# Performance work log

Hardware: AMD Instinct MI355X
Metric: run time of the kernel (lower is better)

## Reference

```python
import jax, jax.numpy as jnp
import numpy as np

N_QUBITS = 12
N_LAYERS = 2
LATENT = 4
BATCH = 8192


def setup_inputs() -> dict:
    key = jax.random.key(0)
    k1, k2, k3, k4, k5, k6 = jax.random.split(key, 6)
    inputs = jax.random.normal(k1, (BATCH, N_QUBITS), jnp.float32)
    q_params = jax.random.normal(k2, (N_LAYERS, N_QUBITS, 3), jnp.float32)
    W1 = jax.random.normal(k3, (32, LATENT), jnp.float32) * 0.3
    b1 = jax.random.normal(k4, (32,), jnp.float32) * 0.1
    W2 = jax.random.normal(k5, (N_QUBITS, 32), jnp.float32) * 0.2
    b2 = jax.random.normal(k6, (N_QUBITS,), jnp.float32) * 0.1
    return {"inputs": inputs, "q_params": q_params, "W1": W1, "b1": b1, "W2": W2, "b2": b2}


def _rot_matrix(phi, theta, omega):
    # PennyLane Rot(phi, theta, omega) = RZ(omega) @ RY(theta) @ RZ(phi)
    c = jnp.cos(theta / 2)
    s = jnp.sin(theta / 2)
    ep = jnp.exp(-0.5j * (phi + omega))  # e^{-i(phi+omega)/2}
    em = jnp.exp(-0.5j * (phi - omega))  # e^{-i(phi-omega)/2}
    row0 = jnp.stack([ep * c, -jnp.conj(em) * s])
    row1 = jnp.stack([em * s, jnp.conj(ep) * c])
    return jnp.stack([row0, row1]).astype(jnp.complex64)  # (2,2)


def _apply_1q(state, U, wire):
    # state: (B,) + (2,)*N_QUBITS ; U: (2,2) shared across batch
    ax = wire + 1
    state = jnp.moveaxis(state, ax, -1)
    state = jnp.einsum('ij,...j->...i', U, state)
    return jnp.moveaxis(state, -1, ax)


def _cnot(state, control, target):
    c_ax, t_ax = control + 1, target + 1
    s0 = jnp.take(state, jnp.array([0]), axis=c_ax)
    s1 = jnp.take(state, jnp.array([1]), axis=c_ax)
    s1 = jnp.flip(s1, axis=t_ax)  # X on target where control==1
    return jnp.concatenate([s0, s1], axis=c_ax)


def _z_expval(state, wire):
    p = state.real ** 2 + state.imag ** 2
    ax = wire + 1
    other = tuple(a for a in range(1, N_QUBITS + 1) if a != ax)
    pw = p.sum(axis=other)  # (B, 2)
    return pw[:, 0] - pw[:, 1]


def reference(inputs, q_params, W1, b1, W2, b2):
    B = inputs.shape[0]
    # Initial |0..0> state followed by per-wire RX(x_i): product state
    # RX(a)|0> = [cos(a/2), -i sin(a/2)]
    c = jnp.cos(inputs / 2).astype(jnp.complex64)  # (B, n)
    s = jnp.sin(inputs / 2).astype(jnp.complex64)
    qvec = jnp.stack([c, -1j * s], axis=-1)  # (B, n, 2)
    state = jnp.ones((B, 1), jnp.complex64)
    for i in range(N_QUBITS):
        state = (state[:, :, None] * qvec[:, i, None, :]).reshape(B, -1)
    state = state.reshape((B,) + (2,) * N_QUBITS)

    for l in range(N_LAYERS):
        for i in range(N_QUBITS):
            phi, theta, omega = q_params[l, i, 0], q_params[l, i, 1], q_params[l, i, 2]
            state = _apply_1q(state, _rot_matrix(phi, theta, omega), i)
        for i in range(N_QUBITS - 1):
            state = _cnot(state, i, i + 1)

    latents = jnp.stack([_z_expval(state, i) for i in range(LATENT)], axis=1)
    latents = latents.astype(jnp.float32)  # (B, latent)

    h = jax.nn.relu(latents @ W1.T + b1)
    return h @ W2.T + b2
```

## Files before the change

kernel.cpp:

```cpp
#include <hip/hip_runtime.h>
#include <hip/hip_bf16.h>


__device__ __forceinline__ void fsincos(float x, float& s, float& c) {
    s = __sinf(x);
    c = __cosf(x);
}

__global__ __launch_bounds__(64) void qae_kernel(
    const float* __restrict__ inputs,
    const float* __restrict__ qp,
    const float* __restrict__ W1,
    const float* __restrict__ b1,
    const float* __restrict__ W2,
    const float* __restrict__ b2,
    float* __restrict__ out,
    int B)
{
    int b = blockIdx.x * blockDim.x + threadIdx.x;
    if (b >= B) return;
    const float* x = inputs + (size_t)b * 12;

    float4 xv = *reinterpret_cast<const float4*>(x);
    float x4 = x[4];

    float cj[5], sj[5];
    fsincos(0.5f * xv.x, sj[0], cj[0]);
    fsincos(0.5f * xv.y, sj[1], cj[1]);
    fsincos(0.5f * xv.z, sj[2], cj[2]);
    fsincos(0.5f * xv.w, sj[3], cj[3]);
    fsincos(0.5f * x4,   sj[4], cj[4]);

    float sr[32], si[32];
#pragma unroll
    for (int idx = 0; idx < 32; ++idx) {
        float m = 1.0f;
#pragma unroll
        for (int j = 0; j < 5; ++j) m *= ((idx >> j) & 1) ? sj[j] : cj[j];
        int pc = __popc(idx) & 3;
        sr[idx] = (pc == 0) ? m : ((pc == 2) ? -m : 0.0f);
        si[idx] = (pc == 1) ? -m : ((pc == 3) ? m : 0.0f);
    }

#pragma unroll
    for (int l = 0; l < 2; ++l) {
#pragma unroll
        for (int w = 0; w < 5; ++w) {
            const float* p = qp + (l * 12 + w) * 3;
            float phi = p[0], th = p[1], om = p[2];
            float st, ct, sha, cha, shb, chb;
            fsincos(0.5f * th, st, ct);
            fsincos(0.5f * (phi + om), sha, cha);
            fsincos(0.5f * (phi - om), shb, chb);
            float u00r =  cha * ct, u00i = -sha * ct;
            float u01r = -chb * st, u01i = -shb * st;
            float u10r =  chb * st, u10i = -shb * st;
            float u11r =  cha * ct, u11i =  sha * ct;
#pragma unroll
            for (int k = 0; k < 16; ++k) {
                int i0 = ((k >> w) << (w + 1)) | (k & ((1 << w) - 1));
                int i1 = i0 | (1 << w);
                float a0r = sr[i0], a0i = si[i0];
                float a1r = sr[i1], a1i = si[i1];
                sr[i0] = u00r * a0r - u00i * a0i + u01r * a1r - u01i * a1i;
                si[i0] = u00r * a0i + u00i * a0r + u01r * a1i + u01i * a1r;
                sr[i1] = u10r * a0r - u10i * a0i + u11r * a1r - u11i * a1i;
                si[i1] = u10r * a0i + u10i * a0r + u11r * a1i + u11i * a1r;
            }
        }
#pragma unroll
        for (int cw = 0; cw < 4; ++cw) {
#pragma unroll
            for (int idx = 0; idx < 32; ++idx) {
                if (((idx >> cw) & 1) && !((idx >> (cw + 1)) & 1)) {
                    int j2 = idx | (1 << (cw + 1));
                    float tr = sr[idx]; sr[idx] = sr[j2]; sr[j2] = tr;
                    float ti = si[idx]; si[idx] = si[j2]; si[j2] = ti;
                }
            }
        }
    }

    float lat[4] = {0.f, 0.f, 0.f, 0.f};
#pragma unroll
    for (int idx = 0; idx < 32; ++idx) {
        float pr = sr[idx] * sr[idx] + si[idx] * si[idx];
#pragma unroll
        for (int q = 0; q < 4; ++q)
            lat[q] += ((idx >> q) & 1) ? -pr : pr;
    }

    float o[12];
#pragma unroll
    for (int j = 0; j < 12; ++j) o[j] = b2[j];
#pragma unroll
    for (int u = 0; u < 32; ++u) {
        float acc = b1[u];
#pragma unroll
        for (int i = 0; i < 4; ++i) acc += lat[i] * W1[u * 4 + i];
        float h = fmaxf(acc, 0.0f);
#pragma unroll
        for (int j = 0; j < 12; ++j) o[j] += h * W2[j * 32 + u];
    }

    float4* op = reinterpret_cast<float4*>(out + (size_t)b * 12);
    op[0] = make_float4(o[0], o[1], o[2], o[3]);
    op[1] = make_float4(o[4], o[5], o[6], o[7]);
    op[2] = make_float4(o[8], o[9], o[10], o[11]);
}

extern "C" void kernel_launch(void* const* d_in, const int* in_sizes, int n_in,
                              void* d_out, int out_size, void* d_ws, size_t ws_size,
                              hipStream_t stream) {
    const float* inputs = (const float*)d_in[0];
    const float* qp     = (const float*)d_in[1];
    const float* W1     = (const float*)d_in[2];
    const float* b1     = (const float*)d_in[3];
    const float* W2     = (const float*)d_in[4];
    const float* b2     = (const float*)d_in[5];
    float* out = (float*)d_out;

    int B = in_sizes[0] / 12;
    int block = 64;
    int grid = (B + block - 1) / block;
    qae_kernel<<<grid, block, 0, stream>>>(inputs, qp, W1, b1, W2, b2, out, B);
}
```

Measured before the change: 76.18 us.

## Split each 32-amplitude statevector across 8 lanes with shuffle-based gates

Each batch element's 32-amplitude reduced state is now distributed over 8 threads holding 4 amplitudes each. Gates on the high wires and the CNOT permutations become cross-lane __shfl_xor exchanges, and the latent reduction and MLP are split across the 8 lanes and combined with shuffle reductions. This cuts per-thread register use and raises the thread count from 8192 to 65536, aiming for better occupancy and latency hiding on a small grid. The cost is many extra shuffles and redundant sincos and parameter work in every lane.

```diff
diff --git a/kernel.cpp b/kernel.cpp
--- a/kernel.cpp
+++ b/kernel.cpp
@@ -7,7 +7,7 @@
     c = __cosf(x);
 }
 
-__global__ __launch_bounds__(64) void qae_kernel(
+__global__ __launch_bounds__(256) void qae_kernel(
     const float* __restrict__ inputs,
     const float* __restrict__ qp,
     const float* __restrict__ W1,
@@ -17,10 +17,12 @@
     float* __restrict__ out,
     int B)
 {
-    int b = blockIdx.x * blockDim.x + threadIdx.x;
-    if (b >= B) return;
-    const float* x = inputs + (size_t)b * 12;
+    int tid = blockIdx.x * blockDim.x + threadIdx.x;
+    int e   = tid >> 3;
+    int sub = tid & 7;
+    if (e >= B) return;
 
+    const float* x = inputs + (size_t)e * 12;
     float4 xv = *reinterpret_cast<const float4*>(x);
     float x4 = x[4];
 
@@ -31,15 +33,27 @@
     fsincos(0.5f * xv.w, sj[3], cj[3]);
     fsincos(0.5f * x4,   sj[4], cj[4]);
 
-    float sr[32], si[32];
+    float fsub = ((sub & 1) ? sj[2] : cj[2])
+               * ((sub & 2) ? sj[3] : cj[3])
+               * ((sub & 4) ? sj[4] : cj[4]);
+
+    float ar[4], ai[4];
 #pragma unroll
-    for (int idx = 0; idx < 32; ++idx) {
-        float m = 1.0f;
-#pragma unroll
-        for (int j = 0; j < 5; ++j) m *= ((idx >> j) & 1) ? sj[j] : cj[j];
-        int pc = __popc(idx) & 3;
-        sr[idx] = (pc == 0) ? m : ((pc == 2) ? -m : 0.0f);
-        si[idx] = (pc == 1) ? -m : ((pc == 3) ? m : 0.0f);
+    for (int r = 0; r < 4; ++r) {
+        float m = fsub * ((r & 1) ? sj[0] : cj[0]) * ((r & 2) ? sj[1] : cj[1]);
+        int pc = (__popc(sub) + __popc(r)) & 3;
+        ar[r] = (pc == 0) ? m : ((pc == 2) ? -m : 0.0f);
+        ai[r] = (pc == 1) ? -m : ((pc == 3) ? m : 0.0f);
+    }
+
+#define APPLY_PAIR(i0, i1)                                        \
+    {                                                             \
+        float a0r = ar[i0], a0i = ai[i0];                         \
+        float a1r = ar[i1], a1i = ai[i1];                         \
+        ar[i0] = u00r*a0r - u00i*a0i + u01r*a1r - u01i*a1i;       \
+        ai[i0] = u00r*a0i + u00i*a0r + u01r*a1i + u01i*a1r;       \
+        ar[i1] = u10r*a0r - u10i*a0i + u11r*a1r - u11i*a1i;       \
+        ai[i1] = u10r*a0i + u10i*a0r + u11r*a1i + u11i*a1r;       \
     }
 
 #pragma unroll
@@ -56,57 +70,102 @@
             float u01r = -chb * st, u01i = -shb * st;
             float u10r =  chb * st, u10i = -shb * st;
             float u11r =  cha * ct, u11i =  sha * ct;
+
+            if (w == 0) {
+                APPLY_PAIR(0, 1);
+                APPLY_PAIR(2, 3);
+            } else if (w == 1) {
+                APPLY_PAIR(0, 2);
+                APPLY_PAIR(1, 3);
+            } else {
+                int lm = 1 << (w - 2);
+                bool hi = (sub >> (w - 2)) & 1;
+                float cmr = hi ? u11r : u00r, cmi = hi ? u11i : u00i;
+                float ctr = hi ? u10r : u01r, cti = hi ? u10i : u01i;
 #pragma unroll
-            for (int k = 0; k < 16; ++k) {
-                int i0 = ((k >> w) << (w + 1)) | (k & ((1 << w) - 1));
-                int i1 = i0 | (1 << w);
-                float a0r = sr[i0], a0i = si[i0];
-                float a1r = sr[i1], a1i = si[i1];
-                sr[i0] = u00r * a0r - u00i * a0i + u01r * a1r - u01i * a1i;
-                si[i0] = u00r * a0i + u00i * a0r + u01r * a1i + u01i * a1r;
-                sr[i1] = u10r * a0r - u10i * a0i + u11r * a1r - u11i * a1i;
-                si[i1] = u10r * a0i + u10i * a0r + u11r * a1i + u11i * a1r;
-            }
-        }
-#pragma unroll
-        for (int cw = 0; cw < 4; ++cw) {
-#pragma unroll
-            for (int idx = 0; idx < 32; ++idx) {
-                if (((idx >> cw) & 1) && !((idx >> (cw + 1)) & 1)) {
-                    int j2 = idx | (1 << (cw + 1));
-                    float tr = sr[idx]; sr[idx] = sr[j2]; sr[j2] = tr;
-                    float ti = si[idx]; si[idx] = si[j2]; si[j2] = ti;
+                for (int r = 0; r < 4; ++r) {
+                    float tr = __shfl_xor(ar[r], lm, 64);
+                    float ti = __shfl_xor(ai[r], lm, 64);
+                    float nr = cmr*ar[r] - cmi*ai[r] + ctr*tr - cti*ti;
+                    float ni = cmr*ai[r] + cmi*ar[r] + ctr*ti + cti*tr;
+                    ar[r] = nr; ai[r] = ni;
                 }
             }
         }
+
+        { float t;
+          t = ar[1]; ar[1] = ar[3]; ar[3] = t;
+          t = ai[1]; ai[1] = ai[3]; ai[3] = t; }
+
+        ar[2] = __shfl_xor(ar[2], 1, 64); ai[2] = __shfl_xor(ai[2], 1, 64);
+        ar[3] = __shfl_xor(ar[3], 1, 64); ai[3] = __shfl_xor(ai[3], 1, 64);
+
+        {
+            bool c = (sub & 1);
+#pragma unroll
+            for (int r = 0; r < 4; ++r) {
+                float tr = __shfl_xor(ar[r], 2, 64);
+                float ti = __shfl_xor(ai[r], 2, 64);
+                if (c) { ar[r] = tr; ai[r] = ti; }
+            }
+        }
+
+        {
+            bool c = (sub & 2);
+#pragma unroll
+            for (int r = 0; r < 4; ++r) {
+                float tr = __shfl_xor(ar[r], 4, 64);
+                float ti = __shfl_xor(ai[r], 4, 64);
+                if (c) { ar[r] = tr; ai[r] = ti; }
+            }
+        }
+    }
+#undef APPLY_PAIR
+
+    float p0 = ar[0]*ar[0] + ai[0]*ai[0];
+    float p1 = ar[1]*ar[1] + ai[1]*ai[1];
+    float p2 = ar[2]*ar[2] + ai[2]*ai[2];
+    float p3 = ar[3]*ar[3] + ai[3]*ai[3];
+    float l0 = p0 - p1 + p2 - p3;
+    float l1 = p0 + p1 - p2 - p3;
+    float sp = p0 + p1 + p2 + p3;
+    float l2 = (sub & 1) ? -sp : sp;
+    float l3 = (sub & 2) ? -sp : sp;
+#pragma unroll
+    for (int m = 1; m <= 4; m <<= 1) {
+        l0 += __shfl_xor(l0, m, 64);
+        l1 += __shfl_xor(l1, m, 64);
+        l2 += __shfl_xor(l2, m, 64);
+        l3 += __shfl_xor(l3, m, 64);
     }
 
-    float lat[4] = {0.f, 0.f, 0.f, 0.f};
+    float4 b1v = reinterpret_cast<const float4*>(b1)[sub];
+    float b1k[4] = {b1v.x, b1v.y, b1v.z, b1v.w};
+    float h[4];
 #pragma unroll
-    for (int idx = 0; idx < 32; ++idx) {
-        float pr = sr[idx] * sr[idx] + si[idx] * si[idx];
+    for (int k = 0; k < 4; ++k) {
+        float4 w = reinterpret_cast<const float4*>(W1)[4 * sub + k];
+        float acc = b1k[k] + l0*w.x + l1*w.y + l2*w.z + l3*w.w;
+        h[k] = fmaxf(acc, 0.0f);
+    }
+    float o[12];
 #pragma unroll
-        for (int q = 0; q < 4; ++q)
-            lat[q] += ((idx >> q) & 1) ? -pr : pr;
+    for (int j = 0; j < 12; ++j) {
+        float4 w2 = *reinterpret_cast<const float4*>(W2 + 32*j + 4*sub);
+        o[j] = h[0]*w2.x + h[1]*w2.y + h[2]*w2.z + h[3]*w2.w;
+    }
+#pragma unroll
+    for (int m = 1; m <= 4; m <<= 1) {
+#pragma unroll
+        for (int j = 0; j < 12; ++j) o[j] += __shfl_xor(o[j], m, 64);
     }
 
-    float o[12];
-#pragma unroll
-    for (int j = 0; j < 12; ++j) o[j] = b2[j];
-#pragma unroll
-    for (int u = 0; u < 32; ++u) {
-        float acc = b1[u];
-#pragma unroll
-        for (int i = 0; i < 4; ++i) acc += lat[i] * W1[u * 4 + i];
-        float h = fmaxf(acc, 0.0f);
-#pragma unroll
-        for (int j = 0; j < 12; ++j) o[j] += h * W2[j * 32 + u];
+    if (sub == 0) {
+        float4* op = reinterpret_cast<float4*>(out + (size_t)e * 12);
+        op[0] = make_float4(o[0]+b2[0], o[1]+b2[1], o[2]+b2[2],  o[3]+b2[3]);
+        op[1] = make_float4(o[4]+b2[4], o[5]+b2[5], o[6]+b2[6],  o[7]+b2[7]);
+        op[2] = make_float4(o[8]+b2[8], o[9]+b2[9], o[10]+b2[10], o[11]+b2[11]);
     }
-
-    float4* op = reinterpret_cast<float4*>(out + (size_t)b * 12);
-    op[0] = make_float4(o[0], o[1], o[2], o[3]);
-    op[1] = make_float4(o[4], o[5], o[6], o[7]);
-    op[2] = make_float4(o[8], o[9], o[10], o[11]);
 }
 
 extern "C" void kernel_launch(void* const* d_in, const int* in_sizes, int n_in,
@@ -121,7 +180,8 @@
     float* out = (float*)d_out;
 
     int B = in_sizes[0] / 12;
-    int block = 64;
-    int grid = (B + block - 1) / block;
+    int threads = B * 8;
+    int block = 256;
+    int grid = (threads + block - 1) / block;
     qae_kernel<<<grid, block, 0, stream>>>(inputs, qp, W1, b1, W2, b2, out, B);
 }
```

Result: faster. 65.62 us (-13.9%).

## Distribute statevector amplitudes across warp lanes with shuffle-based gate application

Applied to the files above, without the earlier changes.

Maps each batch element's 32-amplitude reduced state onto 32 lanes instead of one thread, applying single-qubit rotations and CNOTs via cross-lane shuffles. Rotation matrices are computed once per block into shared memory, and the latent reduction and MLP are parallelized across lanes with a shared-memory hidden buffer. This targets low occupancy and heavy per-thread register use, at the cost of more shuffle traffic and block-level syncs.

```diff
diff --git a/kernel.cpp b/kernel.cpp
--- a/kernel.cpp
+++ b/kernel.cpp
@@ -1,5 +1,4 @@
 #include <hip/hip_runtime.h>
-#include <hip/hip_bf16.h>
 
 
 __device__ __forceinline__ void fsincos(float x, float& s, float& c) {
@@ -7,7 +6,7 @@
     c = __cosf(x);
 }
 
-__global__ __launch_bounds__(64) void qae_kernel(
+__global__ __launch_bounds__(256) void qae_kernel(
     const float* __restrict__ inputs,
     const float* __restrict__ qp,
     const float* __restrict__ W1,
@@ -17,96 +16,106 @@
     float* __restrict__ out,
     int B)
 {
-    int b = blockIdx.x * blockDim.x + threadIdx.x;
-    if (b >= B) return;
-    const float* x = inputs + (size_t)b * 12;
+    __shared__ float ug[10][8];
+    __shared__ float hsh[8][32];
 
+    const int t = threadIdx.x;
+
+    if (t < 10) {
+        int l = t / 5, w = t - 5 * l;
+        const float* p = qp + (l * 12 + w) * 3;
+        float phi = p[0], th = p[1], om = p[2];
+        float st, ct, sha, cha, shb, chb;
+        fsincos(0.5f * th, st, ct);
+        fsincos(0.5f * (phi + om), sha, cha);
+        fsincos(0.5f * (phi - om), shb, chb);
+        ug[t][0] =  cha * ct;  ug[t][1] = -sha * ct;
+        ug[t][2] = -chb * st;  ug[t][3] = -shb * st;
+        ug[t][4] =  chb * st;  ug[t][5] = -shb * st;
+        ug[t][6] =  cha * ct;  ug[t][7] =  sha * ct;
+    }
+
+    const int gtid = blockIdx.x * 256 + t;
+    const int e    = gtid >> 5;
+    const int g    = t & 31;
+    const int eg   = t >> 5;
+    const int ec   = (e < B) ? e : (B - 1);
+
+    const float* x = inputs + (size_t)ec * 12;
     float4 xv = *reinterpret_cast<const float4*>(x);
     float x4 = x[4];
+    float s0,c0,s1,c1,s2,c2,s3,c3,s4,c4;
+    fsincos(0.5f * xv.x, s0, c0);
+    fsincos(0.5f * xv.y, s1, c1);
+    fsincos(0.5f * xv.z, s2, c2);
+    fsincos(0.5f * xv.w, s3, c3);
+    fsincos(0.5f * x4,   s4, c4);
+    float m = ((g & 1) ? s0 : c0) * ((g & 2) ? s1 : c1) * ((g & 4) ? s2 : c2)
+            * ((g & 8) ? s3 : c3) * ((g & 16) ? s4 : c4);
+    int pc = __popc(g) & 3;
+    float ar = (pc == 0) ? m : ((pc == 2) ? -m : 0.0f);
+    float ai = (pc == 1) ? -m : ((pc == 3) ? m : 0.0f);
 
-    float cj[5], sj[5];
-    fsincos(0.5f * xv.x, sj[0], cj[0]);
-    fsincos(0.5f * xv.y, sj[1], cj[1]);
-    fsincos(0.5f * xv.z, sj[2], cj[2]);
-    fsincos(0.5f * xv.w, sj[3], cj[3]);
-    fsincos(0.5f * x4,   sj[4], cj[4]);
-
-    float sr[32], si[32];
-#pragma unroll
-    for (int idx = 0; idx < 32; ++idx) {
-        float m = 1.0f;
-#pragma unroll
-        for (int j = 0; j < 5; ++j) m *= ((idx >> j) & 1) ? sj[j] : cj[j];
-        int pc = __popc(idx) & 3;
-        sr[idx] = (pc == 0) ? m : ((pc == 2) ? -m : 0.0f);
-        si[idx] = (pc == 1) ? -m : ((pc == 3) ? m : 0.0f);
-    }
+    __syncthreads();
 
 #pragma unroll
     for (int l = 0; l < 2; ++l) {
 #pragma unroll
         for (int w = 0; w < 5; ++w) {
-            const float* p = qp + (l * 12 + w) * 3;
-            float phi = p[0], th = p[1], om = p[2];
-            float st, ct, sha, cha, shb, chb;
-            fsincos(0.5f * th, st, ct);
-            fsincos(0.5f * (phi + om), sha, cha);
-            fsincos(0.5f * (phi - om), shb, chb);
-            float u00r =  cha * ct, u00i = -sha * ct;
-            float u01r = -chb * st, u01i = -shb * st;
-            float u10r =  chb * st, u10i = -shb * st;
-            float u11r =  cha * ct, u11i =  sha * ct;
-#pragma unroll
-            for (int k = 0; k < 16; ++k) {
-                int i0 = ((k >> w) << (w + 1)) | (k & ((1 << w) - 1));
-                int i1 = i0 | (1 << w);
-                float a0r = sr[i0], a0i = si[i0];
-                float a1r = sr[i1], a1i = si[i1];
-                sr[i0] = u00r * a0r - u00i * a0i + u01r * a1r - u01i * a1i;
-                si[i0] = u00r * a0i + u00i * a0r + u01r * a1i + u01i * a1r;
-                sr[i1] = u10r * a0r - u10i * a0i + u11r * a1r - u11i * a1i;
-                si[i1] = u10r * a0i + u10i * a0r + u11r * a1i + u11i * a1r;
-            }
+            const float* u = ug[l * 5 + w];
+            float4 ua = *reinterpret_cast<const float4*>(u);
+            float4 ub = *reinterpret_cast<const float4*>(u + 4);
+            bool hi = (g >> w) & 1;
+            float cmr = hi ? ub.z : ua.x;
+            float cmi = hi ? ub.w : ua.y;
+            float ctr = hi ? ub.x : ua.z;
+            float cti = hi ? ub.y : ua.w;
+            float tr = __shfl_xor(ar, 1 << w, 64);
+            float ti = __shfl_xor(ai, 1 << w, 64);
+            float nr = cmr * ar - cmi * ai + ctr * tr - cti * ti;
+            float ni = cmr * ai + cmi * ar + ctr * ti + cti * tr;
+            ar = nr; ai = ni;
         }
 #pragma unroll
-        for (int cw = 0; cw < 4; ++cw) {
-#pragma unroll
-            for (int idx = 0; idx < 32; ++idx) {
-                if (((idx >> cw) & 1) && !((idx >> (cw + 1)) & 1)) {
-                    int j2 = idx | (1 << (cw + 1));
-                    float tr = sr[idx]; sr[idx] = sr[j2]; sr[j2] = tr;
-                    float ti = si[idx]; si[idx] = si[j2]; si[j2] = ti;
-                }
-            }
+        for (int c = 0; c < 4; ++c) {
+            float tr = __shfl_xor(ar, 2 << c, 64);
+            float ti = __shfl_xor(ai, 2 << c, 64);
+            bool ctrl = (g >> c) & 1;
+            ar = ctrl ? tr : ar;
+            ai = ctrl ? ti : ai;
         }
     }
 
-    float lat[4] = {0.f, 0.f, 0.f, 0.f};
+    float p  = ar * ar + ai * ai;
+    float l0 = (g & 1) ? -p : p;
+    float l1 = (g & 2) ? -p : p;
+    float l2 = (g & 4) ? -p : p;
+    float l3 = (g & 8) ? -p : p;
 #pragma unroll
-    for (int idx = 0; idx < 32; ++idx) {
-        float pr = sr[idx] * sr[idx] + si[idx] * si[idx];
-#pragma unroll
-        for (int q = 0; q < 4; ++q)
-            lat[q] += ((idx >> q) & 1) ? -pr : pr;
+    for (int mm = 1; mm <= 16; mm <<= 1) {
+        l0 += __shfl_xor(l0, mm, 64);
+        l1 += __shfl_xor(l1, mm, 64);
+        l2 += __shfl_xor(l2, mm, 64);
+        l3 += __shfl_xor(l3, mm, 64);
     }
 
-    float o[12];
+    float4 w1v = *reinterpret_cast<const float4*>(W1 + 4 * g);
+    float h = fmaxf(b1[g] + l0 * w1v.x + l1 * w1v.y + l2 * w1v.z + l3 * w1v.w, 0.0f);
+    hsh[eg][g] = h;
+    __syncthreads();
+
+    if (e < B && g < 12) {
+        const float4* hv = reinterpret_cast<const float4*>(hsh[eg]);
+        const float4* w2 = reinterpret_cast<const float4*>(W2 + 32 * g);
+        float o = b2[g];
 #pragma unroll
-    for (int j = 0; j < 12; ++j) o[j] = b2[j];
-#pragma unroll
-    for (int u = 0; u < 32; ++u) {
-        float acc = b1[u];
-#pragma unroll
-        for (int i = 0; i < 4; ++i) acc += lat[i] * W1[u * 4 + i];
-        float h = fmaxf(acc, 0.0f);
-#pragma unroll
-        for (int j = 0; j < 12; ++j) o[j] += h * W2[j * 32 + u];
+        for (int k = 0; k < 8; ++k) {
+            float4 hk = hv[k];
+            float4 wk = w2[k];
+            o += hk.x * wk.x + hk.y * wk.y + hk.z * wk.z + hk.w * wk.w;
+        }
+        out[(size_t)e * 12 + g] = o;
     }
-
-    float4* op = reinterpret_cast<float4*>(out + (size_t)b * 12);
-    op[0] = make_float4(o[0], o[1], o[2], o[3]);
-    op[1] = make_float4(o[4], o[5], o[6], o[7]);
-    op[2] = make_float4(o[8], o[9], o[10], o[11]);
 }
 
 extern "C" void kernel_launch(void* const* d_in, const int* in_sizes, int n_in,
@@ -121,7 +130,8 @@
     float* out = (float*)d_out;
 
     int B = in_sizes[0] / 12;
-    int block = 64;
-    int grid = (B + block - 1) / block;
+    long long threads = (long long)B * 32;
+    int block = 256;
+    int grid = (int)((threads + block - 1) / block);
     qae_kernel<<<grid, block, 0, stream>>>(inputs, qp, W1, b1, W2, b2, out, B);
 }
```

Measured after the change: 67.39 us. -11.5%, faster.
